# Performance work log

Measured on AMD Instinct MI355X. Metric: run time of the kernel, lower is better.

The kernel has to match this reference:

```python
import jax, jax.numpy as jnp
import numpy as np

B, S, T = 16, 1024, 512
D, H, L, FF = 256, 8, 4, 1024
DH = D // H  # 32, even (RoPE requirement)


def setup_inputs() -> dict:
    key = jax.random.key(0)
    ks = jax.random.split(key, 8)
    n = lambda k, shape: jax.random.normal(k, shape, dtype=jnp.float32) * 0.02
    return {
        "x": jax.random.normal(ks[0], (B, S, T), dtype=jnp.float32),
        "tok_w": n(ks[1], (D, T)), "tok_b": jnp.zeros((D,), jnp.float32),
        "tnorm_g": jnp.ones((D,), jnp.float32), "tnorm_b": jnp.zeros((D,), jnp.float32),
        "in_proj_w": n(ks[2], (L, 3 * D, D)), "in_proj_b": jnp.zeros((L, 3 * D), jnp.float32),
        "out_w": n(ks[3], (L, D, D)), "out_b": jnp.zeros((L, D), jnp.float32),
        "ln1_g": jnp.ones((L, D), jnp.float32), "ln1_b": jnp.zeros((L, D), jnp.float32),
        "ln2_g": jnp.ones((L, D), jnp.float32), "ln2_b": jnp.zeros((L, D), jnp.float32),
        "lin1_w": n(ks[4], (L, FF, D)), "lin1_b": jnp.zeros((L, FF), jnp.float32),
        "lin2_w": n(ks[5], (L, D, FF)), "lin2_b": jnp.zeros((L, D), jnp.float32),
        "fnorm_g": jnp.ones((D,), jnp.float32), "fnorm_b": jnp.zeros((D,), jnp.float32),
    }


def _ln(x, g, b, eps=1e-5):
    m = x.mean(-1, keepdims=True)
    v = ((x - m) ** 2).mean(-1, keepdims=True)
    return (x - m) * jax.lax.rsqrt(v + eps) * g + b


def _rope_cache():
    half = DH // 2
    inv_freq = 1.0 / (10000.0 ** (jnp.arange(half, dtype=jnp.float32) / half))
    freqs = jnp.arange(S, dtype=jnp.float32)[:, None] * inv_freq[None, :]  # (S, half)
    cos = jnp.concatenate([jnp.cos(freqs), jnp.cos(freqs)], axis=-1)  # (S, DH)
    sin = jnp.concatenate([jnp.sin(freqs), jnp.sin(freqs)], axis=-1)
    return cos[None, None], sin[None, None]  # (1,1,S,DH)


def _rotate_half(x):
    x1, x2 = jnp.split(x, 2, axis=-1)
    return jnp.concatenate([-x2, x1], axis=-1)


def _rope(x, cos, sin):
    return x * cos + _rotate_half(x) * sin


def _encoder(x, tok_w, tok_b, tnorm_g, tnorm_b, in_proj_w, in_proj_b,
             out_w, out_b, ln1_g, ln1_b, ln2_g, ln2_b,
             lin1_w, lin1_b, lin2_w, lin2_b, fnorm_g, fnorm_b):
    # tokenize: Linear(T -> D) per sensor, then LayerNorm
    h = _ln(x @ tok_w.T + tok_b, tnorm_g, tnorm_b)  # (B,S,D)
    cos, sin = _rope_cache()
    scale = 1.0 / np.sqrt(DH).astype(np.float32)
    for i in range(L):
        # --- pre-norm RoPE self-attention ---
        y = _ln(h, ln1_g[i], ln1_b[i])
        qkv = y @ in_proj_w[i].T + in_proj_b[i]  # (B,S,3D)
        q, k, v = jnp.split(qkv, 3, axis=-1)
        q = q.reshape(B, S, H, DH).transpose(0, 2, 1, 3)  # (B,H,S,DH)
        k = k.reshape(B, S, H, DH).transpose(0, 2, 1, 3)
        v = v.reshape(B, S, H, DH).transpose(0, 2, 1, 3)
        q = _rope(q, cos, sin)
        k = _rope(k, cos, sin)
        attn = jax.nn.softmax(jnp.einsum('bhqd,bhkd->bhqk', q, k) * scale, axis=-1)
        o = jnp.einsum('bhqk,bhkd->bhqd', attn, v)
        o = o.transpose(0, 2, 1, 3).reshape(B, S, D)
        h = h + o @ out_w[i].T + out_b[i]
        # --- pre-norm FFN ---
        y2 = _ln(h, ln2_g[i], ln2_b[i])
        h = h + jax.nn.relu(y2 @ lin1_w[i].T + lin1_b[i]) @ lin2_w[i].T + lin2_b[i]
    return _ln(h, fnorm_g, fnorm_b)


def reference(x, tok_w, tok_b, tnorm_g, tnorm_b, in_proj_w, in_proj_b,
              out_w, out_b, ln1_g, ln1_b, ln2_g, ln2_b,
              lin1_w, lin1_b, lin2_w, lin2_b, fnorm_g, fnorm_b):
    return _encoder(x, tok_w, tok_b, tnorm_g, tnorm_b, in_proj_w, in_proj_b,
                    out_w, out_b, ln1_g, ln1_b, ln2_g, ln2_b,
                    lin1_w, lin1_b, lin2_w, lin2_b, fnorm_g, fnorm_b)
```

## Files before the change

kernel.cpp:

```cpp
#include <hip/hip_runtime.h>

#define BB 16
#define SS 1024
#define TT 512
#define DD 256
#define HH 8
#define LL 4
#define FFN 1024
#define DHH 32
#define MROWS (BB*SS)

typedef short bf16x8 __attribute__((ext_vector_type(8)));
typedef float f32x4 __attribute__((ext_vector_type(4)));
typedef float f32x2 __attribute__((ext_vector_type(2)));
typedef unsigned int u32x4 __attribute__((ext_vector_type(4)));

__device__ __forceinline__ unsigned short f2bf(float f) {
    unsigned int u = __float_as_uint(f);
    unsigned int r = (u + 0x7fffu + ((u >> 16) & 1u)) >> 16;
    return (unsigned short)r;
}
__device__ __forceinline__ float bf2f(unsigned short h) {
    return __uint_as_float(((unsigned int)h) << 16);
}
__device__ __forceinline__ unsigned int packbf(float a, float b) {
    return (__float_as_uint(a) >> 16) | (__float_as_uint(b) & 0xffff0000u);
}
__device__ __forceinline__ unsigned int packbf_perm(float p0, float p1) {
    return __builtin_amdgcn_perm(__float_as_uint(p1), __float_as_uint(p0), 0x07060302u);
}

__device__ __forceinline__ void g2l16(const unsigned short* g, unsigned short* l) {
    __builtin_amdgcn_global_load_lds(
        (const __attribute__((address_space(1))) unsigned int*)g,
        (__attribute__((address_space(3))) unsigned int*)l, 16, 0, 0);
}

__global__ __launch_bounds__(256) void convert_weights(
    const float* __restrict__ w0, const float* __restrict__ w1, const float* __restrict__ w2,
    const float* __restrict__ w3, const float* __restrict__ w4, unsigned short* __restrict__ dst)
{
    int i = blockIdx.x * 256 + threadIdx.x;
    if (i >= 3276800) return;
    float v;
    if (i < 131072)        v = w0[i];
    else if (i < 917504)   v = w1[i - 131072];
    else if (i < 1179648)  v = w2[i - 917504];
    else if (i < 2228224)  v = w3[i - 1179648];
    else                   v = w4[i - 2228224];
    dst[i] = f2bf(v);
}

__global__ __launch_bounds__(256) void convert_x(const float4* __restrict__ x, ushort4* __restrict__ xb, int n4)
{
    int i = blockIdx.x * 256 + threadIdx.x;
    if (i >= n4) return;
    float4 v = x[i];
    ushort4 o;
    o.x = f2bf(v.x); o.y = f2bf(v.y); o.z = f2bf(v.z); o.w = f2bf(v.w);
    xb[i] = o;
}

template<int BN, int RELU>
__global__ __launch_bounds__(256, 2) void gemm_lds(
    const unsigned short* __restrict__ A, const unsigned short* __restrict__ Bw,
    const float* __restrict__ bias, void* out, int M, int N, int K)
{
    constexpr int NJ = BN / 32;
    __shared__ __align__(16) unsigned short sA[2][128 * 32];
    __shared__ __align__(16) unsigned short sB[2][BN * 32];
    const int t = threadIdx.x;
    const int lane = t & 63, quad = lane >> 4, l16 = lane & 15;
    const int wave = t >> 6, wm = wave >> 1, wn = wave & 1;
    const int row0 = blockIdx.y * 128, col0 = blockIdx.x * BN;

    const unsigned short* gA = A + (size_t)(row0 + (t >> 2)) * K + (t & 3) * 8;
    const size_t rstep = (size_t)64 * K;
    const unsigned short* gBp[BN / 64];
    #pragma unroll
    for (int p = 0; p < BN / 64; ++p) {
        int l = p * 64 + (t >> 2);
        int wrow = (l & (16 * NJ)) + (l & 15) * NJ + ((l >> 4) & (NJ - 1));
        gBp[p] = Bw + (size_t)(col0 + wrow) * K + (t & 3) * 8;
    }

    f32x4 acc[4][NJ];
    #pragma unroll
    for (int i = 0; i < 4; ++i)
        #pragma unroll
        for (int j = 0; j < NJ; ++j)
            acc[i][j] = (f32x4){0.f, 0.f, 0.f, 0.f};

    g2l16(gA, &sA[0][t * 8]);
    g2l16(gA + rstep, &sA[0][(t + 256) * 8]);
    #pragma unroll
    for (int p = 0; p < BN / 64; ++p)
        g2l16(gBp[p], &sB[0][p * 2048 + t * 8]);

    for (int k0 = 0; k0 < K; k0 += 32) {
        const int cur = (k0 >> 5) & 1;
        __syncthreads();
        if (k0 + 32 < K) {
            const int nxt = cur ^ 1;
            g2l16(gA + k0 + 32, &sA[nxt][t * 8]);
            g2l16(gA + rstep + k0 + 32, &sA[nxt][(t + 256) * 8]);
            #pragma unroll
            for (int p = 0; p < BN / 64; ++p)
                g2l16(gBp[p] + k0 + 32, &sB[nxt][p * 2048 + t * 8]);
        }
        bf16x8 a[4], b[NJ];
        #pragma unroll
        for (int i = 0; i < 4; ++i)
            a[i] = *(const bf16x8*)(&sA[cur][(wm * 64 + i * 16 + l16) * 32 + quad * 8]);
        #pragma unroll
        for (int j = 0; j < NJ; ++j)
            b[j] = *(const bf16x8*)(&sB[cur][(wn * (BN / 2) + j * 16 + l16) * 32 + quad * 8]);
        #pragma unroll
        for (int i = 0; i < 4; ++i)
            #pragma unroll
            for (int j = 0; j < NJ; ++j)
                acc[i][j] = __builtin_amdgcn_mfma_f32_16x16x32_bf16(a[i], b[j], acc[i][j], 0, 0, 0);
    }

    const int colbase = col0 + wn * (BN / 2) + l16 * NJ;
    float bb[NJ];
    #pragma unroll
    for (int j = 0; j < NJ; ++j) bb[j] = bias[colbase + j];
    #pragma unroll
    for (int i = 0; i < 4; ++i) {
        #pragma unroll
        for (int r = 0; r < 4; ++r) {
            int row = row0 + wm * 64 + i * 16 + quad * 4 + r;
            float v[NJ];
            #pragma unroll
            for (int j = 0; j < NJ; ++j) {
                v[j] = acc[i][j][r] + bb[j];
                if (RELU) v[j] = fmaxf(v[j], 0.f);
            }
            unsigned short* dst = (unsigned short*)out + (size_t)row * N + colbase;
            if constexpr (NJ == 4) {
                uint2 w; w.x = packbf(v[0], v[1]); w.y = packbf(v[2], v[3]);
                *(uint2*)dst = w;
            } else {
                uint4 w; w.x = packbf(v[0], v[1]); w.y = packbf(v[2], v[3]);
                w.z = packbf(v[4], v[5]); w.w = packbf(v[6], v[7]);
                *(uint4*)dst = w;
            }
        }
    }
}

__global__ __launch_bounds__(256, 2) void gemm_qkv(
    const unsigned short* __restrict__ A, const unsigned short* __restrict__ Bw,
    const float* __restrict__ bias,
    unsigned short* __restrict__ qr, unsigned short* __restrict__ kr,
    unsigned short* __restrict__ vt)
{
    constexpr int K = 256;
    __shared__ __align__(16) unsigned short sA[2][128 * 32];
    __shared__ __align__(16) unsigned short sB[2][128 * 32];
    __shared__ float scc[128 * 20], scs[128 * 20];
    const int t = threadIdx.x;
    const int lane = t & 63, quad = lane >> 4, l16 = lane & 15;
    const int wave = t >> 6, wm = wave >> 1, wn = wave & 1;
    const int row0 = blockIdx.y * 128, col0 = blockIdx.x * 128;
    const int sec = blockIdx.x >> 1;
    const int b = row0 >> 10, s0 = row0 & 1023;

    if (sec < 2) {
        #pragma unroll
        for (int k = 0; k < 8; ++k) {
            int e = t * 8 + k;
            int rl = e >> 4, jj = e & 15;
            float ivf = __expf(-(float)jj * 0.575646273248511f);
            float c, sn;
            __sincosf((float)(s0 + rl) * ivf, &sn, &c);
            scc[rl * 20 + jj] = c;
            scs[rl * 20 + jj] = sn;
        }
    }

    const unsigned short* gA = A + (size_t)(row0 + (t >> 2)) * K + (t & 3) * 8;
    const size_t rstep = (size_t)64 * K;
    const unsigned short* gBp[2];
    #pragma unroll
    for (int p = 0; p < 2; ++p) {
        int l = p * 64 + (t >> 2);
        int wrow = (l & 64) + (l & 15) * 4 + ((l >> 4) & 3);
        gBp[p] = Bw + (size_t)(col0 + wrow) * K + (t & 3) * 8;
    }

    f32x4 acc[4][4];
    #pragma unroll
    for (int i = 0; i < 4; ++i)
        #pragma unroll
        for (int j = 0; j < 4; ++j)
            acc[i][j] = (f32x4){0.f, 0.f, 0.f, 0.f};

    g2l16(gA, &sA[0][t * 8]);
    g2l16(gA + rstep, &sA[0][(t + 256) * 8]);
    #pragma unroll
    for (int p = 0; p < 2; ++p)
        g2l16(gBp[p], &sB[0][p * 2048 + t * 8]);

    for (int k0 = 0; k0 < K; k0 += 32) {
        const int cur = (k0 >> 5) & 1;
        __syncthreads();
        if (k0 + 32 < K) {
            const int nxt = cur ^ 1;
            g2l16(gA + k0 + 32, &sA[nxt][t * 8]);
            g2l16(gA + rstep + k0 + 32, &sA[nxt][(t + 256) * 8]);
            #pragma unroll
            for (int p = 0; p < 2; ++p)
                g2l16(gBp[p] + k0 + 32, &sB[nxt][p * 2048 + t * 8]);
        }
        bf16x8 a[4], bfr[4];
        #pragma unroll
        for (int i = 0; i < 4; ++i)
            a[i] = *(const bf16x8*)(&sA[cur][(wm * 64 + i * 16 + l16) * 32 + quad * 8]);
        #pragma unroll
        for (int j = 0; j < 4; ++j)
            bfr[j] = *(const bf16x8*)(&sB[cur][(wn * 64 + j * 16 + l16) * 32 + quad * 8]);
        #pragma unroll
        for (int i = 0; i < 4; ++i)
            #pragma unroll
            for (int j = 0; j < 4; ++j)
                acc[i][j] = __builtin_amdgcn_mfma_f32_16x16x32_bf16(a[i], bfr[j], acc[i][j], 0, 0, 0);
    }

    const int gcol = col0 + wn * 64 + l16 * 4;
    const int cc = gcol & 255;
    const int h = cc >> 5, d0v = cc & 31, j0 = d0v & 15;
    const int bh = (b << 3) | h;
    float bbv[4];
    *(float4*)bbv = *(const float4*)(bias + gcol);

    if (sec < 2) {
        const float sgn = ((l16 & 4) == 0) ? -1.f : 1.f;
        const float qs = 1.4426950408889634f / 5.656854249492381f;
        #pragma unroll
        for (int i = 0; i < 4; ++i) {
            #pragma unroll
            for (int r = 0; r < 4; ++r) {
                const int rl = wm * 64 + i * 16 + quad * 4 + r;
                float v0 = acc[i][0][r] + bbv[0];
                float v1 = acc[i][1][r] + bbv[1];
                float v2 = acc[i][2][r] + bbv[2];
                float v3 = acc[i][3][r] + bbv[3];
                float p0 = __shfl_xor(v0, 4);
                float p1 = __shfl_xor(v1, 4);
                float p2 = __shfl_xor(v2, 4);
                float p3 = __shfl_xor(v3, 4);
                float4 cv = *(const float4*)(&scc[rl * 20 + j0]);
                float4 sv = *(const float4*)(&scs[rl * 20 + j0]);
                float o0 = v0 * cv.x + sgn * p0 * sv.x;
                float o1 = v1 * cv.y + sgn * p1 * sv.y;
                float o2 = v2 * cv.z + sgn * p2 * sv.z;
                float o3 = v3 * cv.w + sgn * p3 * sv.w;
                const int s = s0 + rl;
                uint2 w;
                if (sec == 0) {
                    o0 *= qs; o1 *= qs; o2 *= qs; o3 *= qs;
                    w.x = packbf(o0, o1); w.y = packbf(o2, o3);
                    *(uint2*)(qr + ((size_t)bh * SS + s) * DHH + d0v) = w;
                } else {
                    int jj2 = s & 31;
                    int sp = (s & ~31) | (((jj2 & 1) << 4) | (jj2 >> 1));
                    w.x = packbf(o0, o1); w.y = packbf(o2, o3);
                    *(uint2*)(kr + ((size_t)bh * SS + sp) * DHH + d0v) = w;
                }
            }
        }
    } else {
        #pragma unroll
        for (int i = 0; i < 4; ++i) {
            const int sbase = s0 + wm * 64 + i * 16 + quad * 4;
            #pragma unroll
            for (int j = 0; j < 4; ++j) {
                float w0 = acc[i][j][0] + bbv[j];
                float w1 = acc[i][j][1] + bbv[j];
                float w2 = acc[i][j][2] + bbv[j];
                float w3 = acc[i][j][3] + bbv[j];
                uint2 w; w.x = packbf(w0, w1); w.y = packbf(w2, w3);
                *(uint2*)(vt + ((size_t)bh * DHH + d0v + j) * SS + sbase) = w;
            }
        }
    }
}

template<int RESID, int LNH, int YF32>
__global__ __launch_bounds__(256, 2) void gemm_row(
    const unsigned short* __restrict__ A, const unsigned short* __restrict__ Bw,
    const float* __restrict__ bias, const float* __restrict__ resid,
    float* __restrict__ hout, void* __restrict__ yout,
    const float* __restrict__ gh, const float* __restrict__ bh,
    const float* __restrict__ gy, const float* __restrict__ by, int K)
{
    __shared__ __align__(16) unsigned short sA[4][32 * 32];
    __shared__ __align__(16) unsigned short sB[4][256 * 32];
    __shared__ float2 part[2][32][4];
    const int t = threadIdx.x;
    const int quad = (t >> 4) & 3, l16 = t & 15;
    const int wn = t >> 6;
    const int row0 = blockIdx.x * 32;

    const int tq = t & 127, aq = t >> 7;
    const unsigned short* gA = A + (size_t)(row0 + (tq >> 2)) * K + (tq & 3) * 8;
    const unsigned short* gB[4];
    #pragma unroll
    for (int p = 0; p < 4; ++p) {
        int l = p * 64 + (t >> 2);
        gB[p] = Bw + (size_t)((l & 192) + (l & 15) * 4 + ((l >> 4) & 3)) * K + (t & 3) * 8;
    }

    f32x4 acc[2][4];
    #pragma unroll
    for (int i = 0; i < 2; ++i)
        #pragma unroll
        for (int j = 0; j < 4; ++j)
            acc[i][j] = (f32x4){0.f, 0.f, 0.f, 0.f};

    auto stage = [&](int k0, int p) {
        g2l16(gA + k0 + aq * 32, &sA[2 * p + aq][tq * 8]);
        #pragma unroll
        for (int i = 0; i < 4; ++i) {
            g2l16(gB[i] + k0,      &sB[2 * p][i * 2048 + t * 8]);
            g2l16(gB[i] + k0 + 32, &sB[2 * p + 1][i * 2048 + t * 8]);
        }
    };

    stage(0, 0);
    for (int k0 = 0; k0 < K; k0 += 64) {
        const int cur = (k0 >> 6) & 1;
        __syncthreads();
        if (k0 + 64 < K) stage(k0 + 64, cur ^ 1);
        #pragma unroll
        for (int kh = 0; kh < 2; ++kh) {
            bf16x8 a[2], b[4];
            #pragma unroll
            for (int i = 0; i < 2; ++i)
                a[i] = *(const bf16x8*)(&sA[2 * cur + kh][(i * 16 + l16) * 32 + quad * 8]);
            #pragma unroll
            for (int j = 0; j < 4; ++j)
                b[j] = *(const bf16x8*)(&sB[2 * cur + kh][(wn * 64 + j * 16 + l16) * 32 + quad * 8]);
            #pragma unroll
            for (int i = 0; i < 2; ++i)
                #pragma unroll
                for (int j = 0; j < 4; ++j)
                    acc[i][j] = __builtin_amdgcn_mfma_f32_16x16x32_bf16(a[i], b[j], acc[i][j], 0, 0, 0);
        }
    }

    const int colbase = wn * 64 + l16 * 4;
    const float4 bb = *(const float4*)(bias + colbase);
    #pragma unroll
    for (int i = 0; i < 2; ++i) {
        #pragma unroll
        for (int r = 0; r < 4; ++r) {
            const int rl = i * 16 + quad * 4 + r;
            float v0 = acc[i][0][r] + bb.x;
            float v1 = acc[i][1][r] + bb.y;
            float v2 = acc[i][2][r] + bb.z;
            float v3 = acc[i][3][r] + bb.w;
            if (RESID) {
                float4 rv = *(const float4*)(resid + (size_t)(row0 + rl) * DD + colbase);
                v0 += rv.x; v1 += rv.y; v2 += rv.z; v3 += rv.w;
            }
            acc[i][0][r] = v0; acc[i][1][r] = v1; acc[i][2][r] = v2; acc[i][3][r] = v3;
            float s = v0 + v1 + v2 + v3;
            float ss = v0 * v0 + v1 * v1 + v2 * v2 + v3 * v3;
            #pragma unroll
            for (int m = 1; m <= 8; m <<= 1) { s += __shfl_xor(s, m); ss += __shfl_xor(ss, m); }
            if (l16 == 0) part[0][rl][wn] = (float2){s, ss};
        }
    }
    __syncthreads();

    float4 gyv = *(const float4*)(gy + colbase);
    float4 byv = *(const float4*)(by + colbase);
    float4 ghv = {0.f, 0.f, 0.f, 0.f}, bhv = {0.f, 0.f, 0.f, 0.f};
    if (LNH) { ghv = *(const float4*)(gh + colbase); bhv = *(const float4*)(bh + colbase); }

    #pragma unroll
    for (int i = 0; i < 2; ++i) {
        #pragma unroll
        for (int r = 0; r < 4; ++r) {
            const int rl = i * 16 + quad * 4 + r;
            float2 p0 = part[0][rl][0], p1 = part[0][rl][1], p2 = part[0][rl][2], p3 = part[0][rl][3];
            float mean = (p0.x + p1.x + p2.x + p3.x) * (1.f / 256.f);
            float var  = (p0.y + p1.y + p2.y + p3.y) * (1.f / 256.f) - mean * mean;
            float inv  = rsqrtf(var + 1e-5f);
            float h0, h1, h2, h3;
            if (LNH) {
                h0 = (acc[i][0][r] - mean) * inv * ghv.x + bhv.x;
                h1 = (acc[i][1][r] - mean) * inv * ghv.y + bhv.y;
                h2 = (acc[i][2][r] - mean) * inv * ghv.z + bhv.z;
                h3 = (acc[i][3][r] - mean) * inv * ghv.w + bhv.w;
            } else {
                h0 = acc[i][0][r]; h1 = acc[i][1][r]; h2 = acc[i][2][r]; h3 = acc[i][3][r];
            }
            if (!YF32)
                *(float4*)(hout + (size_t)(row0 + rl) * DD + colbase) = (float4){h0, h1, h2, h3};
            if (LNH) {
                acc[i][0][r] = h0; acc[i][1][r] = h1; acc[i][2][r] = h2; acc[i][3][r] = h3;
                float s = h0 + h1 + h2 + h3;
                float ss = h0 * h0 + h1 * h1 + h2 * h2 + h3 * h3;
                #pragma unroll
                for (int m = 1; m <= 8; m <<= 1) { s += __shfl_xor(s, m); ss += __shfl_xor(ss, m); }
                if (l16 == 0) part[1][rl][wn] = (float2){s, ss};
            } else {
                float y0 = (h0 - mean) * inv * gyv.x + byv.x;
                float y1 = (h1 - mean) * inv * gyv.y + byv.y;
                float y2 = (h2 - mean) * inv * gyv.z + byv.z;
                float y3 = (h3 - mean) * inv * gyv.w + byv.w;
                if (YF32) {
                    *(float4*)((float*)yout + (size_t)(row0 + rl) * DD + colbase) = (float4){y0, y1, y2, y3};
                } else {
                    uint2 w; w.x = packbf(y0, y1); w.y = packbf(y2, y3);
                    *(uint2*)((unsigned short*)yout + (size_t)(row0 + rl) * DD + colbase) = w;
                }
            }
        }
    }

    if (LNH) {
        __syncthreads();
        #pragma unroll
        for (int i = 0; i < 2; ++i) {
            #pragma unroll
            for (int r = 0; r < 4; ++r) {
                const int rl = i * 16 + quad * 4 + r;
                float2 p0 = part[1][rl][0], p1 = part[1][rl][1], p2 = part[1][rl][2], p3 = part[1][rl][3];
                float mean = (p0.x + p1.x + p2.x + p3.x) * (1.f / 256.f);
                float var  = (p0.y + p1.y + p2.y + p3.y) * (1.f / 256.f) - mean * mean;
                float inv  = rsqrtf(var + 1e-5f);
                float y0 = (acc[i][0][r] - mean) * inv * gyv.x + byv.x;
                float y1 = (acc[i][1][r] - mean) * inv * gyv.y + byv.y;
                float y2 = (acc[i][2][r] - mean) * inv * gyv.z + byv.z;
                float y3 = (acc[i][3][r] - mean) * inv * gyv.w + byv.w;
                uint2 w; w.x = packbf(y0, y1); w.y = packbf(y2, y3);
                *(uint2*)((unsigned short*)yout + (size_t)(row0 + rl) * DD + colbase) = w;
            }
        }
    }
}

__global__ __launch_bounds__(128, 2) void attn_kernel(
    const unsigned short* __restrict__ qr, const unsigned short* __restrict__ kr,
    const unsigned short* __restrict__ vt, unsigned short* __restrict__ ob)
{
    int t = threadIdx.x;
    int lane = t & 63, wave = t >> 6;
    int quad = (lane >> 4), l16 = lane & 15;
    int bid = blockIdx.x;
    int xcd = bid & 7, jb = bid >> 3;
    int gid = jb * 2 + wave;
    int bh = xcd * 16 + (gid >> 4);
    int q0 = (gid & 15) * 64;
    int b = bh >> 3, h = bh & 7;
    const unsigned short* qbase = qr + ((size_t)bh * SS + q0) * DHH;
    const unsigned short* kbase = kr + (size_t)bh * SS * DHH;
    const unsigned short* vbase = vt + (size_t)bh * DHH * SS;
    bf16x8 qa[4];
    #pragma unroll
    for (int qt = 0; qt < 4; ++qt)
        qa[qt] = *(const bf16x8*)(qbase + (size_t)(qt * 16 + l16) * DHH + quad * 8);
    f32x4 o[4][2] = {};
    f32x2 lsum[4] = {};

    bf16x8 kbA[2][2], vbA[2][2], kbB[2][2], vbB[2][2];

    auto loadKV = [&](int k0, bf16x8 (&kb)[2][2], bf16x8 (&vb)[2][2]) {
        #pragma unroll
        for (int kc = 0; kc < 2; ++kc) {
            const unsigned short* kp = kbase + (size_t)(k0 + kc * 32) * DHH;
            kb[kc][0] = *(const bf16x8*)(kp + (size_t)l16 * DHH + quad * 8);
            kb[kc][1] = *(const bf16x8*)(kp + (size_t)(16 + l16) * DHH + quad * 8);
            vb[kc][0] = *(const bf16x8*)(vbase + (size_t)l16 * SS + k0 + kc * 32 + quad * 8);
            vb[kc][1] = *(const bf16x8*)(vbase + (size_t)(l16 + 16) * SS + k0 + kc * 32 + quad * 8);
        }
    };

    auto tile = [&](bf16x8 (&kb)[2][2], bf16x8 (&vb)[2][2]) {
        __builtin_amdgcn_s_setprio(1);
        #pragma unroll
        for (int qt = 0; qt < 4; ++qt)
            #pragma unroll
            for (int kc = 0; kc < 2; ++kc) {
                f32x4 z = {0.f, 0.f, 0.f, 0.f};
                f32x4 s0 = __builtin_amdgcn_mfma_f32_16x16x32_bf16(kb[kc][0], qa[qt], z, 0, 0, 0);
                f32x4 s1 = __builtin_amdgcn_mfma_f32_16x16x32_bf16(kb[kc][1], qa[qt], z, 0, 0, 0);
                u32x4 pw;
                #pragma unroll
                for (int r = 0; r < 4; ++r) {
                    float p0 = __builtin_amdgcn_exp2f(s0[r]);
                    float p1 = __builtin_amdgcn_exp2f(s1[r]);
                    lsum[qt] += (f32x2){p0, p1};
                    pw[r] = packbf_perm(p0, p1);
                }
                bf16x8 pa = __builtin_bit_cast(bf16x8, pw);
                o[qt][0] = __builtin_amdgcn_mfma_f32_16x16x32_bf16(pa, vb[kc][0], o[qt][0], 0, 0, 0);
                o[qt][1] = __builtin_amdgcn_mfma_f32_16x16x32_bf16(pa, vb[kc][1], o[qt][1], 0, 0, 0);
            }
        __builtin_amdgcn_s_setprio(0);
    };

    loadKV(0, kbA, vbA);
    for (int k0 = 0; k0 < SS; k0 += 128) {
        loadKV(k0 + 64, kbB, vbB);
        tile(kbA, vbA);
        if (k0 + 128 < SS) loadKV(k0 + 128, kbA, vbA);
        tile(kbB, vbB);
    }

    #pragma unroll
    for (int qt = 0; qt < 4; ++qt) {
        float s = lsum[qt][0] + lsum[qt][1];
        s += __shfl_xor(s, 16);
        s += __shfl_xor(s, 32);
        float inv = 1.f / s;
        #pragma unroll
        for (int r = 0; r < 4; ++r) {
            float invr = __shfl(inv, quad * 4 + r);
            int qrow = q0 + qt * 16 + quad * 4 + r;
            size_t base = ((size_t)b * SS + qrow) * DD + h * DHH;
            ob[base + l16]      = f2bf(o[qt][0][r] * invr);
            ob[base + 16 + l16] = f2bf(o[qt][1][r] * invr);
        }
    }
}

extern "C" void kernel_launch(void* const* d_in, const int* in_sizes, int n_in,
                              void* d_out, int out_size, void* d_ws, size_t ws_size,
                              hipStream_t stream)
{
    const float* x        = (const float*)d_in[0];
    const float* tok_w    = (const float*)d_in[1];
    const float* tok_b    = (const float*)d_in[2];
    const float* tnorm_g  = (const float*)d_in[3];
    const float* tnorm_b  = (const float*)d_in[4];
    const float* in_proj_w= (const float*)d_in[5];
    const float* in_proj_b= (const float*)d_in[6];
    const float* out_w    = (const float*)d_in[7];
    const float* out_b    = (const float*)d_in[8];
    const float* ln1_g    = (const float*)d_in[9];
    const float* ln1_b    = (const float*)d_in[10];
    const float* ln2_g    = (const float*)d_in[11];
    const float* ln2_b    = (const float*)d_in[12];
    const float* lin1_w   = (const float*)d_in[13];
    const float* lin1_b   = (const float*)d_in[14];
    const float* lin2_w   = (const float*)d_in[15];
    const float* lin2_b   = (const float*)d_in[16];
    const float* fnorm_g  = (const float*)d_in[17];
    const float* fnorm_b  = (const float*)d_in[18];

    char* ws = (char*)d_ws;
    unsigned short* wb        = (unsigned short*)ws;
    unsigned short* wb_tok    = wb;
    unsigned short* wb_inproj = wb + 131072;
    unsigned short* wb_out    = wb + 917504;
    unsigned short* wb_lin1   = wb + 1179648;
    unsigned short* wb_lin2   = wb + 2228224;
    unsigned short* xb   = (unsigned short*)(ws + 6553600);
    float*          h    = (float*)(ws + 31719424);
    unsigned short* y    = (unsigned short*)(ws + 48496640);
    unsigned short* qr   = (unsigned short*)(ws + 56885248);
    unsigned short* kr   = (unsigned short*)(ws + 65273856);
    unsigned short* vt   = (unsigned short*)(ws + 73662464);
    unsigned short* ob   = (unsigned short*)(ws + 82051072);
    unsigned short* a1   = (unsigned short*)(ws + 90439680);

    convert_weights<<<dim3(12800), dim3(256), 0, stream>>>(tok_w, in_proj_w, out_w, lin1_w, lin2_w, wb);
    convert_x<<<dim3(8192), dim3(256), 0, stream>>>((const float4*)x, (ushort4*)xb, MROWS * TT / 4);

    gemm_row<0, 1, 0><<<dim3(MROWS / 32), dim3(256), 0, stream>>>(
        xb, wb_tok, tok_b, nullptr, h, y, tnorm_g, tnorm_b, ln1_g, ln1_b, TT);

    for (int i = 0; i < LL; ++i) {
        gemm_qkv<<<dim3(6, MROWS / 128), dim3(256), 0, stream>>>(
            y, wb_inproj + (size_t)i * 3 * DD * DD, in_proj_b + i * 3 * DD, qr, kr, vt);
        attn_kernel<<<dim3(1024), dim3(128), 0, stream>>>(qr, kr, vt, ob);
        gemm_row<1, 0, 0><<<dim3(MROWS / 32), dim3(256), 0, stream>>>(
            ob, wb_out + (size_t)i * DD * DD, out_b + i * DD, h, h, y,
            nullptr, nullptr, ln2_g + i * DD, ln2_b + i * DD, DD);
        gemm_lds<256, 1><<<dim3(FFN / 256, MROWS / 128), dim3(256), 0, stream>>>(
            y, wb_lin1 + (size_t)i * FFN * DD, lin1_b + i * FFN, a1, MROWS, FFN, DD);
        if (i < LL - 1) {
            gemm_row<1, 0, 0><<<dim3(MROWS / 32), dim3(256), 0, stream>>>(
                a1, wb_lin2 + (size_t)i * DD * FFN, lin2_b + i * DD, h, h, y,
                nullptr, nullptr, ln1_g + (i + 1) * DD, ln1_b + (i + 1) * DD, FFN);
        } else {
            gemm_row<1, 0, 1><<<dim3(MROWS / 32), dim3(256), 0, stream>>>(
                a1, wb_lin2 + (size_t)i * DD * FFN, lin2_b + i * DD, h, h, d_out,
                nullptr, nullptr, fnorm_g, fnorm_b, FFN);
        }
    }
}
```

Baseline: 545.7 us.

## Split attention keys across two waves per block and combine via LDS

Each block now processes a single 64-query tile, with its two waves each covering half of the key sequence. Wave 1 writes its partial output accumulators and row sums to shared memory, and wave 0 adds them and normalizes. The grid is doubled so there are twice as many waves, which is meant to improve occupancy and latency hiding in the attention kernel. This adds an LDS exchange, a barrier, and an idle wave during the epilogue.

New measurement: 560.7 us. +2.8%, slower.

```diff
diff --git a/kernel.cpp b/kernel.cpp
--- a/kernel.cpp
+++ b/kernel.cpp
@@ -449,15 +449,16 @@
     const unsigned short* __restrict__ qr, const unsigned short* __restrict__ kr,
     const unsigned short* __restrict__ vt, unsigned short* __restrict__ ob)
 {
+    __shared__ float comb[64][37];
     int t = threadIdx.x;
     int lane = t & 63, wave = t >> 6;
     int quad = (lane >> 4), l16 = lane & 15;
     int bid = blockIdx.x;
     int xcd = bid & 7, jb = bid >> 3;
-    int gid = jb * 2 + wave;
-    int bh = xcd * 16 + (gid >> 4);
-    int q0 = (gid & 15) * 64;
+    int bh = xcd * 16 + (jb >> 4);
+    int q0 = (jb & 15) * 64;
     int b = bh >> 3, h = bh & 7;
+    const int kbeg = wave * 512;
     const unsigned short* qbase = qr + ((size_t)bh * SS + q0) * DHH;
     const unsigned short* kbase = kr + (size_t)bh * SS * DHH;
     const unsigned short* vbase = vt + (size_t)bh * DHH * SS;
@@ -505,27 +506,46 @@
         __builtin_amdgcn_s_setprio(0);
     };
 
-    loadKV(0, kbA, vbA);
-    for (int k0 = 0; k0 < SS; k0 += 128) {
+    loadKV(kbeg, kbA, vbA);
+    for (int k0 = kbeg; k0 < kbeg + 512; k0 += 128) {
         loadKV(k0 + 64, kbB, vbB);
         tile(kbA, vbA);
-        if (k0 + 128 < SS) loadKV(k0 + 128, kbA, vbA);
+        if (k0 + 128 < kbeg + 512) loadKV(k0 + 128, kbA, vbA);
         tile(kbB, vbB);
     }
 
-    #pragma unroll
-    for (int qt = 0; qt < 4; ++qt) {
-        float s = lsum[qt][0] + lsum[qt][1];
-        s += __shfl_xor(s, 16);
-        s += __shfl_xor(s, 32);
-        float inv = 1.f / s;
-        #pragma unroll
-        for (int r = 0; r < 4; ++r) {
-            float invr = __shfl(inv, quad * 4 + r);
-            int qrow = q0 + qt * 16 + quad * 4 + r;
-            size_t base = ((size_t)b * SS + qrow) * DD + h * DHH;
-            ob[base + l16]      = f2bf(o[qt][0][r] * invr);
-            ob[base + 16 + l16] = f2bf(o[qt][1][r] * invr);
+    if (wave == 1) {
+        #pragma unroll
+        for (int qt = 0; qt < 4; ++qt) {
+            #pragma unroll
+            for (int j = 0; j < 2; ++j)
+                #pragma unroll
+                for (int r = 0; r < 4; ++r)
+                    comb[lane][qt * 8 + j * 4 + r] = o[qt][j][r];
+            comb[lane][32 + qt] = lsum[qt][0] + lsum[qt][1];
+        }
+    }
+    __syncthreads();
+    if (wave == 0) {
+        #pragma unroll
+        for (int qt = 0; qt < 4; ++qt) {
+            #pragma unroll
+            for (int j = 0; j < 2; ++j)
+                #pragma unroll
+                for (int r = 0; r < 4; ++r)
+                    o[qt][j][r] += comb[lane][qt * 8 + j * 4 + r];
+            float s = lsum[qt][0] + lsum[qt][1] + comb[lane][32 + qt];
+            s += __shfl_xor(s, 16);
+            s += __shfl_xor(s, 32);
+            float inv = 1.f / s;
+            #pragma unroll
+            for (int r = 0; r < 4; ++r) {
+                float invr = __shfl(inv, quad * 4 + r);
+                int qrow = q0 + qt * 16 + quad * 4 + r;
+                size_t base = ((size_t)b * SS + qrow) * DD + h * DHH;
+                ob[base + l16]      = f2bf(o[qt][0][r] * invr);
+                ob[base + 16 + l16] = f2bf(o[qt][1][r] * invr);
+            }
         }
     }
 }
@@ -579,7 +599,7 @@
     for (int i = 0; i < LL; ++i) {
         gemm_qkv<<<dim3(6, MROWS / 128), dim3(256), 0, stream>>>(
             y, wb_inproj + (size_t)i * 3 * DD * DD, in_proj_b + i * 3 * DD, qr, kr, vt);
-        attn_kernel<<<dim3(1024), dim3(128), 0, stream>>>(qr, kr, vt, ob);
+        attn_kernel<<<dim3(2048), dim3(128), 0, stream>>>(qr, kr, vt, ob);
         gemm_row<1, 0, 0><<<dim3(MROWS / 32), dim3(256), 0, stream>>>(
             ob, wb_out + (size_t)i * DD * DD, out_b + i * DD, h, h, y,
             nullptr, nullptr, ln2_g + i * DD, ln2_b + i * DD, DD);
```
